# Performance work log

Hardware: AMD Instinct MI355X
Metric: run time of the kernel (lower is better)

The kernel has to match this reference:

```python
import jax, jax.numpy as jnp
import numpy as np

IN_FEATURES = 4096
OUT_FEATURES = 4096
BATCH, SEQ = 8, 2048


def setup_inputs() -> dict:
    key = jax.random.key(0)
    k_in, k_w, k_b = jax.random.split(key, 3)
    inputs = {
        "input": jax.random.normal(k_in, (BATCH, SEQ, IN_FEATURES), dtype=jnp.float32),
        # int8-valued weights stored as int32 (range [-128, 127])
        "quantized_weight": jax.random.randint(k_w, (OUT_FEATURES, IN_FEATURES), -128, 128, dtype=jnp.int32),
        "weight_scale": jnp.array([0.01], dtype=jnp.float32),
        "weight_zero_point": jnp.array([2], dtype=jnp.int32),
        # int16-valued bias stored as int32 (range [-32768, 32767])
        "quantized_bias": jax.random.randint(k_b, (OUT_FEATURES,), -32768, 32768, dtype=jnp.int32),
        "bias_scale": jnp.array([0.0005], dtype=jnp.float32),
        "bias_zero_point": jnp.array([1], dtype=jnp.int32),
    }
    return inputs


def reference(input, quantized_weight, weight_scale, weight_zero_point,
              quantized_bias, bias_scale, bias_zero_point) -> jnp.ndarray:
    # Dequantize weights: (q - zp) * scale  -> [out, in] fp32
    w = (quantized_weight.astype(jnp.float32) - weight_zero_point.astype(jnp.float32)) * weight_scale
    # Dequantize bias -> [out] fp32
    b = (quantized_bias.astype(jnp.float32) - bias_zero_point.astype(jnp.float32)) * bias_scale
    # F.linear: input @ w.T + b ; input [B, S, in] -> out [B, S, out]
    return jnp.einsum('bsi,oi->bso', input, w) + b
```

## Files before the change

kernel.cpp:

```cpp
#include <hip/hip_runtime.h>

#define M_DIM 16384
#define N_DIM 4096
#define K_DIM 4096
#define BK 64
#define NKT (K_DIM / BK)

typedef unsigned char u8;
typedef __attribute__((ext_vector_type(4))) int   i32x4;
typedef __attribute__((ext_vector_type(4))) float f32x4;

#define AS1 __attribute__((address_space(1)))
#define AS3 __attribute__((address_space(3)))

__global__ __launch_bounds__(256)
void quant_a_kernel(const float* __restrict__ in, char* __restrict__ out,
                    float* __restrict__ srow, int* __restrict__ rsum) {
    const int row  = blockIdx.x;
    const int t    = threadIdx.x;
    const int lane = t & 63, wv = t >> 6;
    const float4* rp = (const float4*)(in + (size_t)row * K_DIM);

    float4 v[4];
#pragma unroll
    for (int j = 0; j < 4; ++j) v[j] = rp[t + 256 * j];

    float amax = 0.f;
#pragma unroll
    for (int j = 0; j < 4; ++j) {
        amax = fmaxf(amax, fmaxf(fmaxf(fabsf(v[j].x), fabsf(v[j].y)),
                                 fmaxf(fabsf(v[j].z), fabsf(v[j].w))));
    }
#pragma unroll
    for (int off = 32; off; off >>= 1) amax = fmaxf(amax, __shfl_xor(amax, off));
    __shared__ float wred[4];
    __shared__ int   sred[4];
    if (lane == 0) wred[wv] = amax;
    __syncthreads();
    amax = fmaxf(fmaxf(wred[0], wred[1]), fmaxf(wred[2], wred[3]));
    const float inv = amax > 0.f ? 127.f / amax : 0.f;

    int lsum = 0;
    unsigned* orow = (unsigned*)(out + (size_t)row * K_DIM);
#pragma unroll
    for (int j = 0; j < 4; ++j) {
        int q0 = __float2int_rn(v[j].x * inv);
        int q1 = __float2int_rn(v[j].y * inv);
        int q2 = __float2int_rn(v[j].z * inv);
        int q3 = __float2int_rn(v[j].w * inv);
        lsum += q0 + q1 + q2 + q3;
        unsigned pk = (unsigned)(q0 & 0xFF) | ((unsigned)(q1 & 0xFF) << 8) |
                      ((unsigned)(q2 & 0xFF) << 16) | ((unsigned)(q3 & 0xFF) << 24);
        orow[t + 256 * j] = pk;
    }
#pragma unroll
    for (int off = 32; off; off >>= 1) lsum += __shfl_xor(lsum, off);
    if (lane == 0) sred[wv] = lsum;
    __syncthreads();
    if (t == 0) {
        rsum[row] = sred[0] + sred[1] + sred[2] + sred[3];
        srow[row] = amax > 0.f ? amax / 127.f : 1.f;
    }
}

__global__ __launch_bounds__(256)
void pack_w_kernel(const int* __restrict__ q, char* __restrict__ out, int n4) {
    int stride = gridDim.x * blockDim.x;
    for (int i = blockIdx.x * blockDim.x + threadIdx.x; i < n4; i += stride) {
        int4 a = ((const int4*)q)[i];
        unsigned pk = (unsigned)(a.x & 0xFF) | ((unsigned)(a.y & 0xFF) << 8) |
                      ((unsigned)(a.z & 0xFF) << 16) | ((unsigned)(a.w & 0xFF) << 24);
        ((unsigned*)out)[i] = pk;
    }
}

__global__ __launch_bounds__(512, 2)
void gemm_i8_kernel(const char* __restrict__ A, const char* __restrict__ B,
                    const float* __restrict__ srow, const int* __restrict__ rsum,
                    const float* __restrict__ wsc_p, const int* __restrict__ wzp_p,
                    const int* __restrict__ qb, const float* __restrict__ bsc_p,
                    const int* __restrict__ bzp_p, float* __restrict__ C) {
    __shared__ __align__(16) u8 lds[4 * 32768];

    const int nwg = gridDim.x;
    const int cpx = nwg >> 3;
    const int bid = blockIdx.x;
    const int swz = (bid & 7) * cpx + (bid >> 3);
    const int st = swz >> 5, wi = swz & 31;
    const int bm = (st >> 2) * 8 + (wi >> 2);
    const int bn = (st & 3) * 4 + (wi & 3);
    const int m0 = bm * 256, n0 = bn * 256;

    const int tid  = threadIdx.x;
    const int wv   = tid >> 6;
    const int lane = tid & 63;
    const int wr   = wv >> 2;
    const int wcn  = wv & 3;
    const int l15  = lane & 15;

    const int koff = (((lane >> 4) ^ ((lane >> 1) & 3)) << 4);

    const int srt  = tid >> 2;
    const int gcol = (((tid & 3) ^ ((tid >> 3) & 3)) << 4);
    const char* AgT = A + (size_t)(m0 + srt) * K_DIM + gcol;
    const char* BgT = B + (size_t)(n0 + srt) * K_DIM + gcol;
    const int wvo = wv << 10;

    i32x4 acc[8][4] = {};

    auto STAGE_A = [&](int ns, int k3) {
#pragma unroll
        for (int i = 0; i < 2; ++i)
            __builtin_amdgcn_global_load_lds(
                (const AS1 void*)(AgT + (size_t)i * 128 * K_DIM + k3),
                (AS3 void*)(lds + ns * 32768 + i * 8192 + wvo), 16, 0, 0);
    };
    auto STAGE_B = [&](int ns, int k3) {
#pragma unroll
        for (int i = 0; i < 2; ++i)
            __builtin_amdgcn_global_load_lds(
                (const AS1 void*)(BgT + (size_t)i * 128 * K_DIM + k3),
                (AS3 void*)(lds + ns * 32768 + 16384 + i * 8192 + wvo), 16, 0, 0);
    };

    STAGE_A(0, 0);      STAGE_B(0, 0);
    STAGE_A(1, BK);     STAGE_B(1, BK);
    STAGE_A(2, 2 * BK); STAGE_B(2, 2 * BK);
    asm volatile("s_waitcnt vmcnt(8)" ::: "memory");
    __builtin_amdgcn_s_barrier();
    __builtin_amdgcn_sched_barrier(0);

#pragma unroll 4
    for (int u = 0; u < NKT; ++u) {
        const int cs = u & 3;
        const u8* Asl = lds + cs * 32768;
        const u8* Bsl = Asl + 16384;
        const bool pf = (u + 3) < NKT;
        const int ns = (u + 3) & 3;
        const int k3 = (u + 3) * BK;

        i32x4 af[8], bfr[4];

#pragma unroll
        for (int mi = 0; mi < 8; ++mi) {
            int row = wr * 128 + mi * 16 + l15;
            af[mi] = *(const i32x4*)(Asl + row * 64 + koff);
        }
#pragma unroll
        for (int ni = 0; ni < 4; ++ni) {
            int row = wcn * 64 + ni * 16 + l15;
            bfr[ni] = *(const i32x4*)(Bsl + row * 64 + koff);
        }
        if (pf) { STAGE_A(ns, k3); STAGE_B(ns, k3); }

        asm volatile("s_waitcnt lgkmcnt(0)" ::: "memory");
        __builtin_amdgcn_sched_barrier(0);
        __builtin_amdgcn_s_setprio(1);
#pragma unroll
        for (int mi = 0; mi < 8; ++mi)
#pragma unroll
            for (int ni = 0; ni < 4; ++ni)
                acc[mi][ni] = __builtin_amdgcn_mfma_i32_16x16x64_i8(
                    af[mi], bfr[ni], acc[mi][ni], 0, 0, 0);
        __builtin_amdgcn_s_setprio(0);

        if (u < NKT - 3)       asm volatile("s_waitcnt vmcnt(8)" ::: "memory");
        else if (u == NKT - 3) asm volatile("s_waitcnt vmcnt(4)" ::: "memory");
        else if (u == NKT - 2) asm volatile("s_waitcnt vmcnt(0)" ::: "memory");
        __builtin_amdgcn_s_barrier();
        __builtin_amdgcn_sched_barrier(0);
    }

    const float ws  = wsc_p[0];
    const float zpf = (float)wzp_p[0];
    const float bsc = bsc_p[0];
    const float bzp = (float)bzp_p[0];
    float bias_[4];
#pragma unroll
    for (int ni = 0; ni < 4; ++ni) {
        int col = n0 + wcn * 64 + ni * 16 + l15;
        bias_[ni] = ((float)qb[col] - bzp) * bsc;
    }
#pragma unroll
    for (int mi = 0; mi < 8; ++mi) {
        int rbase = m0 + wr * 128 + mi * 16 + (lane >> 4) * 4;
        float fs_[4], fc_[4];
#pragma unroll
        for (int i = 0; i < 4; ++i) {
            float sf = ws * srow[rbase + i];
            fs_[i] = sf;
            fc_[i] = -sf * zpf * (float)rsum[rbase + i];
        }
#pragma unroll
        for (int ni = 0; ni < 4; ++ni) {
            int col = n0 + wcn * 64 + ni * 16 + l15;
#pragma unroll
            for (int i = 0; i < 4; ++i)
                C[(size_t)(rbase + i) * N_DIM + col] =
                    fs_[i] * (float)acc[mi][ni][i] + fc_[i] + bias_[ni];
        }
    }
}

__global__ void gemm_fallback_kernel(const float* __restrict__ A, const int* __restrict__ Wq,
                                     const float* __restrict__ wsc_p, const int* __restrict__ wzp_p,
                                     const int* __restrict__ qb, const float* __restrict__ bsc_p,
                                     const int* __restrict__ bzp_p, float* __restrict__ C) {
    int m = blockIdx.y;
    int n = blockIdx.x * 256 + threadIdx.x;
    float zp = (float)wzp_p[0];
    float sc = wsc_p[0];
    __shared__ float Arow[512];
    float acc = 0.f;
    for (int k0 = 0; k0 < K_DIM; k0 += 512) {
        __syncthreads();
        for (int t = threadIdx.x; t < 512; t += 256)
            Arow[t] = A[(size_t)m * K_DIM + k0 + t];
        __syncthreads();
        const int4* wp = (const int4*)(Wq + (size_t)n * K_DIM + k0);
        for (int kk = 0; kk < 512; kk += 4) {
            int4 q = wp[kk >> 2];
            acc += Arow[kk]     * ((float)q.x - zp);
            acc += Arow[kk + 1] * ((float)q.y - zp);
            acc += Arow[kk + 2] * ((float)q.z - zp);
            acc += Arow[kk + 3] * ((float)q.w - zp);
        }
    }
    acc *= sc;
    acc += ((float)qb[n] - (float)bzp_p[0]) * bsc_p[0];
    C[(size_t)m * N_DIM + n] = acc;
}

extern "C" void kernel_launch(void* const* d_in, const int* in_sizes, int n_in,
                              void* d_out, int out_size, void* d_ws, size_t ws_size,
                              hipStream_t stream) {
    (void)in_sizes; (void)n_in; (void)out_size;
    const float* input = (const float*)d_in[0];
    const int*   qw    = (const int*)d_in[1];
    const float* wsc   = (const float*)d_in[2];
    const int*   wzp   = (const int*)d_in[3];
    const int*   qb    = (const int*)d_in[4];
    const float* bsc   = (const float*)d_in[5];
    const int*   bzp   = (const int*)d_in[6];
    float* out = (float*)d_out;

    size_t offA = 0;
    size_t offW = (size_t)M_DIM * K_DIM;
    size_t offS = offW + (size_t)N_DIM * K_DIM;
    size_t offR = offS + (size_t)M_DIM * sizeof(float);
    size_t need = offR + (size_t)M_DIM * sizeof(int);

    if (ws_size >= need) {
        char*  Aq = (char*)d_ws + offA;
        char*  Wq8 = (char*)d_ws + offW;
        float* S  = (float*)((char*)d_ws + offS);
        int*   R  = (int*)((char*)d_ws + offR);
        quant_a_kernel<<<M_DIM, 256, 0, stream>>>(input, Aq, S, R);
        pack_w_kernel<<<2048, 256, 0, stream>>>(qw, Wq8, N_DIM * K_DIM / 4);
        gemm_i8_kernel<<<(M_DIM / 256) * (N_DIM / 256), 512, 0, stream>>>(
            Aq, Wq8, S, R, wsc, wzp, qb, bsc, bzp, out);
    } else {
        dim3 grid(N_DIM / 256, M_DIM);
        gemm_fallback_kernel<<<grid, 256, 0, stream>>>(input, qw, wsc, wzp, qb, bsc, bzp, out);
    }
}
```

Baseline: 378.9 us.

## Use 4-wave 128x128 warp tiles with ping-pong B fragments overlapping LDS reads and MFMA

Cuts the int8 GEMM workgroup from 8 waves to 4, so each wave computes a 128x128 output tile (8x8 MFMA accumulators) instead of 128x64. The A fragments are split into two halves and B fragments are double-buffered in registers, so LDS reads for the next half and tile are issued while MFMAs run on the previous ones. The goal is more operand reuse per LDS read and better hiding of LDS latency behind MFMA. In exchange, register pressure rises sharply (256 accumulator registers plus fragments) and there are fewer waves per CU to hide latency.

Result: faster. 369.8 us (-2.4%).

```diff
diff --git a/kernel.cpp b/kernel.cpp
--- a/kernel.cpp
+++ b/kernel.cpp
@@ -8,7 +8,6 @@
 
 typedef unsigned char u8;
 typedef __attribute__((ext_vector_type(4))) int   i32x4;
-typedef __attribute__((ext_vector_type(4))) float f32x4;
 
 #define AS1 __attribute__((address_space(1)))
 #define AS3 __attribute__((address_space(3)))
@@ -74,7 +73,7 @@
     }
 }
 
-__global__ __launch_bounds__(512, 2)
+__global__ __launch_bounds__(256, 1)
 void gemm_i8_kernel(const char* __restrict__ A, const char* __restrict__ B,
                     const float* __restrict__ srow, const int* __restrict__ rsum,
                     const float* __restrict__ wsc_p, const int* __restrict__ wzp_p,
@@ -94,8 +93,8 @@
     const int tid  = threadIdx.x;
     const int wv   = tid >> 6;
     const int lane = tid & 63;
-    const int wr   = wv >> 2;
-    const int wcn  = wv & 3;
+    const int wr   = wv >> 1;
+    const int wcn  = wv & 1;
     const int l15  = lane & 15;
 
     const int koff = (((lane >> 4) ^ ((lane >> 1) & 3)) << 4);
@@ -106,79 +105,109 @@
     const char* BgT = B + (size_t)(n0 + srt) * K_DIM + gcol;
     const int wvo = wv << 10;
 
-    i32x4 acc[8][4] = {};
-
-    auto STAGE_A = [&](int ns, int k3) {
-#pragma unroll
-        for (int i = 0; i < 2; ++i)
+    i32x4 acc[8][8] = {};
+    i32x4 afA[4], afB[4], bfrP[8], bfrQ[8];
+
+    auto STAGE_AB = [&](int ns, int k3) {
+#pragma unroll
+        for (int i = 0; i < 4; ++i)
             __builtin_amdgcn_global_load_lds(
-                (const AS1 void*)(AgT + (size_t)i * 128 * K_DIM + k3),
-                (AS3 void*)(lds + ns * 32768 + i * 8192 + wvo), 16, 0, 0);
+                (const AS1 void*)(AgT + (size_t)i * 64 * K_DIM + k3),
+                (AS3 void*)(lds + ns * 32768 + i * 4096 + wvo), 16, 0, 0);
+#pragma unroll
+        for (int i = 0; i < 4; ++i)
+            __builtin_amdgcn_global_load_lds(
+                (const AS1 void*)(BgT + (size_t)i * 64 * K_DIM + k3),
+                (AS3 void*)(lds + ns * 32768 + 16384 + i * 4096 + wvo), 16, 0, 0);
     };
-    auto STAGE_B = [&](int ns, int k3) {
-#pragma unroll
-        for (int i = 0; i < 2; ++i)
-            __builtin_amdgcn_global_load_lds(
-                (const AS1 void*)(BgT + (size_t)i * 128 * K_DIM + k3),
-                (AS3 void*)(lds + ns * 32768 + 16384 + i * 8192 + wvo), 16, 0, 0);
-    };
-
-    STAGE_A(0, 0);      STAGE_B(0, 0);
-    STAGE_A(1, BK);     STAGE_B(1, BK);
-    STAGE_A(2, 2 * BK); STAGE_B(2, 2 * BK);
-    asm volatile("s_waitcnt vmcnt(8)" ::: "memory");
+
+#define READ_AFA(ASL)                                                          \
+    _Pragma("unroll")                                                          \
+    for (int mi = 0; mi < 4; ++mi)                                             \
+        afA[mi] = *(const i32x4*)((ASL) + (wr * 128 + mi * 16 + l15) * 64 + koff);
+#define READ_AFB(ASL)                                                          \
+    _Pragma("unroll")                                                          \
+    for (int mi = 0; mi < 4; ++mi)                                             \
+        afB[mi] = *(const i32x4*)((ASL) + (wr * 128 + 64 + mi * 16 + l15) * 64 + koff);
+#define READ_BFR(BSL, BARR)                                                    \
+    _Pragma("unroll")                                                          \
+    for (int ni = 0; ni < 8; ++ni)                                             \
+        BARR[ni] = *(const i32x4*)((BSL) + (wcn * 128 + ni * 16 + l15) * 64 + koff);
+#define MFMA_C1(BARR)                                                          \
+    __builtin_amdgcn_s_setprio(1);                                             \
+    _Pragma("unroll")                                                          \
+    for (int mi = 0; mi < 4; ++mi)                                             \
+        _Pragma("unroll")                                                      \
+        for (int ni = 0; ni < 8; ++ni)                                         \
+            acc[mi][ni] = __builtin_amdgcn_mfma_i32_16x16x64_i8(               \
+                afA[mi], BARR[ni], acc[mi][ni], 0, 0, 0);                      \
+    __builtin_amdgcn_s_setprio(0);
+#define MFMA_C2(BARR)                                                          \
+    __builtin_amdgcn_s_setprio(1);                                             \
+    _Pragma("unroll")                                                          \
+    for (int mi = 0; mi < 4; ++mi)                                             \
+        _Pragma("unroll")                                                      \
+        for (int ni = 0; ni < 8; ++ni)                                         \
+            acc[mi + 4][ni] = __builtin_amdgcn_mfma_i32_16x16x64_i8(           \
+                afB[mi], BARR[ni], acc[mi + 4][ni], 0, 0, 0);                  \
+    __builtin_amdgcn_s_setprio(0);
+
+#define TILE_BODY(U, BCUR, BPREV)                                              \
+    do {                                                                       \
+        const int u_ = (U);                                                    \
+        const u8* Asl_ = lds + (u_ & 3) * 32768;                               \
+        const u8* Bsl_ = Asl_ + 16384;                                         \
+        READ_AFA(Asl_)                                                         \
+        READ_BFR(Bsl_, BCUR)                                                   \
+        if (u_ + 3 < NKT) STAGE_AB((u_ + 3) & 3, (u_ + 3) * BK);               \
+        MFMA_C2(BPREV)                                                         \
+        MFMA_C1(BCUR)                                                          \
+        READ_AFB(Asl_)                                                         \
+        asm volatile("s_waitcnt lgkmcnt(0)" ::: "memory");                     \
+        if (u_ < NKT - 3)       asm volatile("s_waitcnt vmcnt(16)" ::: "memory"); \
+        else if (u_ == NKT - 3) asm volatile("s_waitcnt vmcnt(8)" ::: "memory");  \
+        else if (u_ == NKT - 2) asm volatile("s_waitcnt vmcnt(0)" ::: "memory");  \
+        __builtin_amdgcn_s_barrier();                                          \
+        __builtin_amdgcn_sched_barrier(0);                                     \
+    } while (0)
+
+    STAGE_AB(0, 0);
+    STAGE_AB(1, BK);
+    STAGE_AB(2, 2 * BK);
+    asm volatile("s_waitcnt vmcnt(16)" ::: "memory");
     __builtin_amdgcn_s_barrier();
     __builtin_amdgcn_sched_barrier(0);
 
-#pragma unroll 4
-    for (int u = 0; u < NKT; ++u) {
-        const int cs = u & 3;
-        const u8* Asl = lds + cs * 32768;
-        const u8* Bsl = Asl + 16384;
-        const bool pf = (u + 3) < NKT;
-        const int ns = (u + 3) & 3;
-        const int k3 = (u + 3) * BK;
-
-        i32x4 af[8], bfr[4];
-
-#pragma unroll
-        for (int mi = 0; mi < 8; ++mi) {
-            int row = wr * 128 + mi * 16 + l15;
-            af[mi] = *(const i32x4*)(Asl + row * 64 + koff);
-        }
-#pragma unroll
-        for (int ni = 0; ni < 4; ++ni) {
-            int row = wcn * 64 + ni * 16 + l15;
-            bfr[ni] = *(const i32x4*)(Bsl + row * 64 + koff);
-        }
-        if (pf) { STAGE_A(ns, k3); STAGE_B(ns, k3); }
-
+    {
+        const u8* Asl_ = lds;
+        const u8* Bsl_ = Asl_ + 16384;
+        READ_AFA(Asl_)
+        READ_BFR(Bsl_, bfrP)
+        STAGE_AB(3, 3 * BK);
+        MFMA_C1(bfrP)
+        READ_AFB(Asl_)
         asm volatile("s_waitcnt lgkmcnt(0)" ::: "memory");
-        __builtin_amdgcn_sched_barrier(0);
-        __builtin_amdgcn_s_setprio(1);
-#pragma unroll
-        for (int mi = 0; mi < 8; ++mi)
-#pragma unroll
-            for (int ni = 0; ni < 4; ++ni)
-                acc[mi][ni] = __builtin_amdgcn_mfma_i32_16x16x64_i8(
-                    af[mi], bfr[ni], acc[mi][ni], 0, 0, 0);
-        __builtin_amdgcn_s_setprio(0);
-
-        if (u < NKT - 3)       asm volatile("s_waitcnt vmcnt(8)" ::: "memory");
-        else if (u == NKT - 3) asm volatile("s_waitcnt vmcnt(4)" ::: "memory");
-        else if (u == NKT - 2) asm volatile("s_waitcnt vmcnt(0)" ::: "memory");
+        asm volatile("s_waitcnt vmcnt(16)" ::: "memory");
         __builtin_amdgcn_s_barrier();
         __builtin_amdgcn_sched_barrier(0);
     }
+
+    for (int v = 1; v < NKT - 1; v += 2) {
+        TILE_BODY(v,     bfrQ, bfrP);
+        TILE_BODY(v + 1, bfrP, bfrQ);
+    }
+    TILE_BODY(NKT - 1, bfrQ, bfrP);
+
+    MFMA_C2(bfrQ)
 
     const float ws  = wsc_p[0];
     const float zpf = (float)wzp_p[0];
     const float bsc = bsc_p[0];
     const float bzp = (float)bzp_p[0];
-    float bias_[4];
-#pragma unroll
-    for (int ni = 0; ni < 4; ++ni) {
-        int col = n0 + wcn * 64 + ni * 16 + l15;
+    float bias_[8];
+#pragma unroll
+    for (int ni = 0; ni < 8; ++ni) {
+        int col = n0 + wcn * 128 + ni * 16 + l15;
         bias_[ni] = ((float)qb[col] - bzp) * bsc;
     }
 #pragma unroll
@@ -192,14 +221,20 @@
             fc_[i] = -sf * zpf * (float)rsum[rbase + i];
         }
 #pragma unroll
-        for (int ni = 0; ni < 4; ++ni) {
-            int col = n0 + wcn * 64 + ni * 16 + l15;
+        for (int ni = 0; ni < 8; ++ni) {
+            int col = n0 + wcn * 128 + ni * 16 + l15;
 #pragma unroll
             for (int i = 0; i < 4; ++i)
                 C[(size_t)(rbase + i) * N_DIM + col] =
                     fs_[i] * (float)acc[mi][ni][i] + fc_[i] + bias_[ni];
         }
     }
+#undef TILE_BODY
+#undef MFMA_C1
+#undef MFMA_C2
+#undef READ_AFA
+#undef READ_AFB
+#undef READ_BFR
 }
 
 __global__ void gemm_fallback_kernel(const float* __restrict__ A, const int* __restrict__ Wq,
@@ -257,7 +292,7 @@
         int*   R  = (int*)((char*)d_ws + offR);
         quant_a_kernel<<<M_DIM, 256, 0, stream>>>(input, Aq, S, R);
         pack_w_kernel<<<2048, 256, 0, stream>>>(qw, Wq8, N_DIM * K_DIM / 4);
-        gemm_i8_kernel<<<(M_DIM / 256) * (N_DIM / 256), 512, 0, stream>>>(
+        gemm_i8_kernel<<<(M_DIM / 256) * (N_DIM / 256), 256, 0, stream>>>(
             Aq, Wq8, S, R, wsc, wzp, qb, bsc, bzp, out);
     } else {
         dim3 grid(N_DIM / 256, M_DIM);
```
